# Kernel optimization log

Measured on AMD Instinct MI355X. Metric: run time of the kernel, lower is better.

The kernel has to match this reference:

```python
import jax, jax.numpy as jnp
import numpy as np

N = 8192       # tokens (batch*seq)
D = 4096       # input_size / d_model
H = 256        # gate hidden_size
E = 64         # num_experts
K = 2          # top_k


def setup_inputs() -> dict:
    key = jax.random.key(0)
    k0, k1, k2, k3 = jax.random.split(key, 4)
    x = jax.random.normal(k0, (N, D), dtype=jnp.float32)
    # nn.Linear default init: U(-1/sqrt(fan_in), 1/sqrt(fan_in))
    w1 = jax.random.uniform(k1, (H, D), jnp.float32, -1.0, 1.0) / np.sqrt(D)
    b1 = jax.random.uniform(k2, (H,), jnp.float32, -1.0, 1.0) / np.sqrt(D)
    w2 = jax.random.uniform(k3, (E, H), jnp.float32, -1.0, 1.0) / np.sqrt(H)
    return {"x": x, "w1": w1, "b1": b1, "w2": w2}


def reference(x, w1, b1, w2):
    # MLP gate: Linear -> GELU (exact erf, torch default) -> Dropout(eval: identity) -> Linear(no bias)
    h = jax.nn.gelu(jnp.einsum('nd,hd->nh', x, w1) + b1, approximate=False)  # [N, H]
    logits = jnp.einsum('nh,eh->ne', h, w2)                                  # [N, E]
    probs = jax.nn.softmax(logits, axis=-1)                                  # [N, E]
    # deterministic top-k path (sample_topk=0 / eval mode)
    top_k_gates, top_k_indices = jax.lax.top_k(probs, K)                     # [N, K] each
    return top_k_indices, top_k_gates, probs
```

## Files before the change

### kernel.cpp

```cpp
#include <hip/hip_runtime.h>
#include <hip/hip_bf16.h>
#include <math.h>

#define NTOK 8192
#define DIN  4096
#define HG   256
#define NE   64
#define SPLITK 4
#define KSTEPS 32
#define TR   16

typedef __attribute__((ext_vector_type(8))) short short8;
typedef __attribute__((ext_vector_type(4))) short short4v;
typedef __attribute__((ext_vector_type(4))) float f32x4;

__device__ __forceinline__ unsigned short f2bf_rne(float f) {
    union { float f; unsigned int u; } v; v.f = f;
    unsigned int r = v.u + 0x7fffu + ((v.u >> 16) & 1u);
    return (unsigned short)(r >> 16);
}
__device__ __forceinline__ float bf2f(unsigned short b) {
    union { unsigned int u; float f; } v; v.u = ((unsigned int)b) << 16;
    return v.f;
}

typedef const __attribute__((address_space(1))) unsigned int* gptr_t;
typedef __attribute__((address_space(3))) unsigned int* lptr_t;
__device__ __forceinline__ void gload_lds16(const void* g, void* l) {
    __builtin_amdgcn_global_load_lds((gptr_t)g, (lptr_t)l, 16, 0, 0);
}

__global__ __launch_bounds__(512) void convert_w1_kernel(
    const float* __restrict__ w1, unsigned short* __restrict__ w1t)
{
    const int id    = blockIdx.x * 512 + threadIdx.x;
    const int lane  = id & 63;
    const int cg    = id >> 6;
    const int kstep = cg >> 5;
    const int c     = cg & 31;
    const int hl    = c >> 4;
    const int unit  = c & 15;
    const int n     = unit * 16 + (lane & 15);
    const int k     = kstep * 32 + ((lane >> 4) & 3) * 8;

    const float* src = w1 + (size_t)n * DIN + k;
    short8 v;
#pragma unroll
    for (int j = 0; j < 8; ++j) {
        float f = src[j];
        unsigned short hi = f2bf_rne(f);
        v[j] = (hl == 0) ? (short)hi : (short)f2bf_rne(f - bf2f(hi));
    }
    *(short8*)(w1t + (size_t)cg * 512 + lane * 8) = v;
}

__global__ __launch_bounds__(256, 2) void gemm1_mfma_kernel(
    const float* __restrict__ x, const unsigned short* __restrict__ w1t,
    float* __restrict__ P)
{
    __shared__ unsigned short As[2][2][4][512];
    __shared__ unsigned short Bs[2][2][16][512];

    const int bid  = blockIdx.x;
    const int mblk = bid & 127;
    const int s    = bid >> 7;
    const int t    = threadIdx.x;
    const int lane = t & 63;
    const int w    = t >> 6;

    const int m_base = mblk * 64;
    const int kstep0 = s * KSTEPS;

    const int a_unit = t >> 6;
    const int a_q    = t & 63;
    const int a_row  = a_unit * 16 + (a_q & 15);
    const int a_koff = (a_q >> 4) * 8;
    const float* asrc = x + (size_t)(m_base + a_row) * DIN
                          + (size_t)kstep0 * 32 + a_koff;
    const int a_ldso = a_q * 8;

    f32x4 acc[4][4];
#pragma unroll
    for (int i = 0; i < 4; ++i)
#pragma unroll
        for (int j = 0; j < 4; ++j) acc[i][j] = (f32x4)0.f;

#define CVT8_STORE(BUF, F0, F1)                                               \
    {   short8 vh_, vl_;                                                      \
        float ff_[8] = { (F0).x, (F0).y, (F0).z, (F0).w,                      \
                         (F1).x, (F1).y, (F1).z, (F1).w };                    \
        _Pragma("unroll")                                                     \
        for (int j_ = 0; j_ < 8; ++j_) {                                      \
            unsigned short h_ = f2bf_rne(ff_[j_]);                            \
            vh_[j_] = (short)h_;                                              \
            vl_[j_] = (short)f2bf_rne(ff_[j_] - bf2f(h_));                    \
        }                                                                     \
        *(short8*)&As[BUF][0][a_unit][a_ldso] = vh_;                          \
        *(short8*)&As[BUF][1][a_unit][a_ldso] = vl_;                          \
    }

#pragma unroll
    for (int i = 0; i < 8; ++i) {
        const int c = w * 8 + i;
        gload_lds16(w1t + ((size_t)kstep0 * 32 + c) * 512 + lane * 8,
                    &Bs[0][c >> 4][c & 15][0]);
    }
    {
        float4 a0 = *(const float4*)(asrc);
        float4 a1 = *(const float4*)(asrc + 4);
        CVT8_STORE(0, a0, a1)
    }
    __syncthreads();

#pragma unroll 1
    for (int tt = 0; tt < KSTEPS; ++tt) {
        const int bcur = tt & 1, bnxt = bcur ^ 1;
        const bool last = (tt == KSTEPS - 1);

        float4 nx0, nx1;
        if (!last) {
            const float* ap = asrc + (size_t)(tt + 1) * 32;
            nx0 = *(const float4*)(ap);
            nx1 = *(const float4*)(ap + 4);
#pragma unroll
            for (int i = 0; i < 8; ++i) {
                const int c = w * 8 + i;
                gload_lds16(w1t + ((size_t)(kstep0 + tt + 1) * 32 + c) * 512 + lane * 8,
                            &Bs[bnxt][c >> 4][c & 15][0]);
            }
        }

        short8 ahf[4], alf[4], bhf[4], blf[4];
#pragma unroll
        for (int mr = 0; mr < 4; ++mr) {
            ahf[mr] = *(const short8*)&As[bcur][0][mr][lane * 8];
            alf[mr] = *(const short8*)&As[bcur][1][mr][lane * 8];
        }
#pragma unroll
        for (int nr = 0; nr < 4; ++nr) {
            bhf[nr] = *(const short8*)&Bs[bcur][0][w * 4 + nr][lane * 8];
            blf[nr] = *(const short8*)&Bs[bcur][1][w * 4 + nr][lane * 8];
        }

#pragma unroll
        for (int mr = 0; mr < 4; ++mr)
#pragma unroll
            for (int nr = 0; nr < 4; ++nr)
                acc[mr][nr] = __builtin_amdgcn_mfma_f32_16x16x32_bf16(
                    ahf[mr], bhf[nr], acc[mr][nr], 0, 0, 0);
#pragma unroll
        for (int mr = 0; mr < 4; ++mr)
#pragma unroll
            for (int nr = 0; nr < 4; ++nr)
                acc[mr][nr] = __builtin_amdgcn_mfma_f32_16x16x32_bf16(
                    ahf[mr], blf[nr], acc[mr][nr], 0, 0, 0);
#pragma unroll
        for (int mr = 0; mr < 4; ++mr)
#pragma unroll
            for (int nr = 0; nr < 4; ++nr)
                acc[mr][nr] = __builtin_amdgcn_mfma_f32_16x16x32_bf16(
                    alf[mr], bhf[nr], acc[mr][nr], 0, 0, 0);

        if (!last) {
            CVT8_STORE(bnxt, nx0, nx1)
            __syncthreads();
        }
    }
#undef CVT8_STORE

    float* pb = P + (size_t)s * ((size_t)NTOK * HG);
#pragma unroll
    for (int mr = 0; mr < 4; ++mr)
#pragma unroll
        for (int nr = 0; nr < 4; ++nr) {
            const int n = w * 64 + nr * 16 + (lane & 15);
#pragma unroll
            for (int r = 0; r < 4; ++r) {
                const int m = m_base + mr * 16 + ((lane >> 4) & 3) * 4 + r;
                pb[(size_t)m * HG + n] = acc[mr][nr][r];
            }
        }
}

__global__ __launch_bounds__(512, 4) void reduce_gate_kernel(
    const float* __restrict__ P, const float* __restrict__ b1,
    const float* __restrict__ w2, float* __restrict__ out)
{
    __shared__ float h_lds[TR][260];
    __shared__ float lg[NE][33];

    const int t    = threadIdx.x;
    const int lane = t & 63;
    const int w    = t >> 6;
    const int r0   = blockIdx.x * TR;
    const size_t SS = (size_t)NTOK * HG;

    {
        const int row = t >> 5;
        const int sg  = t & 31;
        const size_t base = (size_t)(r0 + row) * HG + sg * 8;

        float q[8];
#pragma unroll
        for (int half = 0; half < 2; ++half) {
            float4 v0 = *(const float4*)(P + base + half * 4);
            float4 v1 = *(const float4*)(P + base + SS + half * 4);
            float4 v2 = *(const float4*)(P + base + 2 * SS + half * 4);
            float4 v3 = *(const float4*)(P + base + 3 * SS + half * 4);
            float4 bb = *(const float4*)(b1 + sg * 8 + half * 4);
            q[half * 4 + 0] = v0.x + v1.x + v2.x + v3.x + bb.x;
            q[half * 4 + 1] = v0.y + v1.y + v2.y + v3.y + bb.y;
            q[half * 4 + 2] = v0.z + v1.z + v2.z + v3.z + bb.z;
            q[half * 4 + 3] = v0.w + v1.w + v2.w + v3.w + bb.w;
        }
#pragma unroll
        for (int c = 0; c < 8; ++c)
            q[c] = 0.5f * q[c] * (1.0f + erff(q[c] * 0.70710678118654752440f));

        *(float4*)&h_lds[row][sg * 8]     = make_float4(q[0], q[1], q[2], q[3]);
        *(float4*)&h_lds[row][sg * 8 + 4] = make_float4(q[4], q[5], q[6], q[7]);
    }
    __syncthreads();

    const int e0   = w * 8;
    const int rowp = lane & 15;
    const int kq   = lane >> 4;

    float acc[8];
#pragma unroll
    for (int i = 0; i < 8; ++i) acc[i] = 0.f;

    const float* w2b = w2 + (size_t)e0 * HG + kq * 64;
#pragma unroll 1
    for (int kc = 0; kc < 64; kc += 8) {
        float a[8];
        *(float4*)&a[0] = *(const float4*)&h_lds[rowp][kq * 64 + kc];
        *(float4*)&a[4] = *(const float4*)&h_lds[rowp][kq * 64 + kc + 4];
#pragma unroll
        for (int n = 0; n < 8; ++n) {
            const float* wr = w2b + (size_t)n * HG + kc;
            float4 w0 = *(const float4*)(wr);
            float4 w1v = *(const float4*)(wr + 4);
            acc[n] = fmaf(w0.x, a[0], acc[n]);
            acc[n] = fmaf(w0.y, a[1], acc[n]);
            acc[n] = fmaf(w0.z, a[2], acc[n]);
            acc[n] = fmaf(w0.w, a[3], acc[n]);
            acc[n] = fmaf(w1v.x, a[4], acc[n]);
            acc[n] = fmaf(w1v.y, a[5], acc[n]);
            acc[n] = fmaf(w1v.z, a[6], acc[n]);
            acc[n] = fmaf(w1v.w, a[7], acc[n]);
        }
    }
#pragma unroll
    for (int n = 0; n < 8; ++n) {
        acc[n] += __shfl_xor(acc[n], 16);
        acc[n] += __shfl_xor(acc[n], 32);
    }
    if (lane < 16) {
#pragma unroll
        for (int n = 0; n < 8; ++n) lg[e0 + n][rowp] = acc[n];
    }
    __syncthreads();

    if (t < TR) {
        float l[NE];
#pragma unroll
        for (int e = 0; e < NE; ++e) l[e] = lg[e][t];

        float mx = l[0];
#pragma unroll
        for (int e = 1; e < NE; ++e) mx = fmaxf(mx, l[e]);

        float ssum = 0.f;
#pragma unroll
        for (int e = 0; e < NE; ++e) { float p = expf(l[e] - mx); l[e] = p; ssum += p; }
        const float inv = 1.0f / ssum;
#pragma unroll
        for (int e = 0; e < NE; ++e) l[e] *= inv;

        float v1 = -1.0f, v2 = -2.0f;
        int   i1 = 0,     i2 = 0;
#pragma unroll
        for (int e = 0; e < NE; ++e) {
            const float p  = l[e];
            const bool  g1 = p > v1;
            const bool  g2 = p > v2;
            const float nv2 = g1 ? v1 : (g2 ? p : v2);
            const int   ni2 = g1 ? i1 : (g2 ? e : i2);
            v1 = g1 ? p : v1;
            i1 = g1 ? e : i1;
            v2 = nv2;
            i2 = ni2;
        }

        const int row = r0 + t;
        float* out_idx  = out;
        float* out_gate = out + 2 * NTOK;
        float* out_prob = out + 4 * NTOK;
        out_idx[2 * row + 0]  = (float)i1;
        out_idx[2 * row + 1]  = (float)i2;
        out_gate[2 * row + 0] = v1;
        out_gate[2 * row + 1] = v2;

        float* pr = out_prob + (size_t)row * NE;
#pragma unroll
        for (int e = 0; e < NE; e += 4)
            *(float4*)(pr + e) = make_float4(l[e], l[e + 1], l[e + 2], l[e + 3]);
    }
}

extern "C" void kernel_launch(void* const* d_in, const int* in_sizes, int n_in,
                              void* d_out, int out_size, void* d_ws, size_t ws_size,
                              hipStream_t stream) {
    const float* x  = (const float*)d_in[0];
    const float* w1 = (const float*)d_in[1];
    const float* b1 = (const float*)d_in[2];
    const float* w2 = (const float*)d_in[3];
    float* out = (float*)d_out;

    unsigned short* w1t = (unsigned short*)d_ws;
    float* P = (float*)((char*)d_ws + (4u << 20));

    convert_w1_kernel<<<512, 512, 0, stream>>>(w1, w1t);
    gemm1_mfma_kernel<<<512, 256, 0, stream>>>(x, w1t, P);
    reduce_gate_kernel<<<512, 512, 0, stream>>>(P, b1, w2, out);
}
```

Before: 91.77 us.

## Enlarge GEMM1 tile to 128 rows with 8 waves and triple-buffered W1 prefetch

The first GEMM now uses 512-thread blocks covering 128 token rows, so each W1 tile loaded into LDS feeds twice as many rows and B traffic drops. W1 tiles are triple-buffered and prefetched two k-steps ahead, with explicit vmcnt waits and raw barriers in place of __syncthreads. Blocks are remapped so neighbouring blocks share a split-K slice, and MFMA sections run at raised wave priority. The cost is more LDS per block and half as many blocks (256), which may reduce occupancy and latency hiding on a device with many CUs.

```diff
diff --git a/kernel.cpp b/kernel.cpp
--- a/kernel.cpp
+++ b/kernel.cpp
@@ -11,7 +11,6 @@
 #define TR   16
 
 typedef __attribute__((ext_vector_type(8))) short short8;
-typedef __attribute__((ext_vector_type(4))) short short4v;
 typedef __attribute__((ext_vector_type(4))) float f32x4;
 
 __device__ __forceinline__ unsigned short f2bf_rne(float f) {
@@ -29,6 +28,13 @@
 __device__ __forceinline__ void gload_lds16(const void* g, void* l) {
     __builtin_amdgcn_global_load_lds((gptr_t)g, (lptr_t)l, 16, 0, 0);
 }
+
+#define WAIT_VMCNT4 { asm volatile("s_waitcnt vmcnt(4)" ::: "memory"); \
+                      __builtin_amdgcn_sched_barrier(0); }
+#define WAIT_VMCNT0 { asm volatile("s_waitcnt vmcnt(0)" ::: "memory"); \
+                      __builtin_amdgcn_sched_barrier(0); }
+#define WAIT_LGKM0  { asm volatile("s_waitcnt lgkmcnt(0)" ::: "memory"); \
+                      __builtin_amdgcn_sched_barrier(0); }
 
 __global__ __launch_bounds__(512) void convert_w1_kernel(
     const float* __restrict__ w1, unsigned short* __restrict__ w1t)
@@ -54,21 +60,23 @@
     *(short8*)(w1t + (size_t)cg * 512 + lane * 8) = v;
 }
 
-__global__ __launch_bounds__(256, 2) void gemm1_mfma_kernel(
+__global__ __launch_bounds__(512, 2) void gemm1_mfma_kernel(
     const float* __restrict__ x, const unsigned short* __restrict__ w1t,
     float* __restrict__ P)
 {
-    __shared__ unsigned short As[2][2][4][512];
-    __shared__ unsigned short Bs[2][2][16][512];
+    __shared__ unsigned short As[2][2][8][512];
+    __shared__ unsigned short Bs[3][2][16][512];
 
     const int bid  = blockIdx.x;
-    const int mblk = bid & 127;
-    const int s    = bid >> 7;
+    const int s    = (bid & 7) >> 1;
+    const int mblk = ((bid >> 3) << 1) | (bid & 1);
     const int t    = threadIdx.x;
     const int lane = t & 63;
     const int w    = t >> 6;
-
-    const int m_base = mblk * 64;
+    const int wm   = w >> 2;
+    const int wn   = w & 3;
+
+    const int m_base = mblk * 128;
     const int kstep0 = s * KSTEPS;
 
     const int a_unit = t >> 6;
@@ -99,49 +107,54 @@
         *(short8*)&As[BUF][1][a_unit][a_ldso] = vl_;                          \
     }
 
-#pragma unroll
-    for (int i = 0; i < 8; ++i) {
-        const int c = w * 8 + i;
-        gload_lds16(w1t + ((size_t)kstep0 * 32 + c) * 512 + lane * 8,
-                    &Bs[0][c >> 4][c & 15][0]);
-    }
+#define ISSUE_B(KS, BUF)                                                      \
+    _Pragma("unroll")                                                         \
+    for (int i_ = 0; i_ < 4; ++i_) {                                          \
+        const int c_ = w * 4 + i_;                                            \
+        gload_lds16(w1t + ((size_t)(KS) * 32 + c_) * 512 + lane * 8,          \
+                    &Bs[BUF][c_ >> 4][c_ & 15][0]);                           \
+    }
+
     {
         float4 a0 = *(const float4*)(asrc);
         float4 a1 = *(const float4*)(asrc + 4);
+        ISSUE_B(kstep0, 0)
         CVT8_STORE(0, a0, a1)
-    }
-    __syncthreads();
+        ISSUE_B(kstep0 + 1, 1)
+        WAIT_VMCNT4
+        WAIT_LGKM0
+        __builtin_amdgcn_s_barrier();
+    }
+
+    int bcur = 0, bnx1 = 1, bnx2 = 2;
+    int acur = 0;
 
 #pragma unroll 1
     for (int tt = 0; tt < KSTEPS; ++tt) {
-        const int bcur = tt & 1, bnxt = bcur ^ 1;
-        const bool last = (tt == KSTEPS - 1);
+        const bool has1 = (tt + 1 < KSTEPS);
+        const bool has2 = (tt + 2 < KSTEPS);
 
         float4 nx0, nx1;
-        if (!last) {
+        if (has1) {
             const float* ap = asrc + (size_t)(tt + 1) * 32;
             nx0 = *(const float4*)(ap);
             nx1 = *(const float4*)(ap + 4);
-#pragma unroll
-            for (int i = 0; i < 8; ++i) {
-                const int c = w * 8 + i;
-                gload_lds16(w1t + ((size_t)(kstep0 + tt + 1) * 32 + c) * 512 + lane * 8,
-                            &Bs[bnxt][c >> 4][c & 15][0]);
-            }
-        }
+        }
+        if (has2) { ISSUE_B(kstep0 + tt + 2, bnx2) }
 
         short8 ahf[4], alf[4], bhf[4], blf[4];
 #pragma unroll
         for (int mr = 0; mr < 4; ++mr) {
-            ahf[mr] = *(const short8*)&As[bcur][0][mr][lane * 8];
-            alf[mr] = *(const short8*)&As[bcur][1][mr][lane * 8];
+            ahf[mr] = *(const short8*)&As[acur][0][wm * 4 + mr][lane * 8];
+            alf[mr] = *(const short8*)&As[acur][1][wm * 4 + mr][lane * 8];
         }
 #pragma unroll
         for (int nr = 0; nr < 4; ++nr) {
-            bhf[nr] = *(const short8*)&Bs[bcur][0][w * 4 + nr][lane * 8];
-            blf[nr] = *(const short8*)&Bs[bcur][1][w * 4 + nr][lane * 8];
-        }
-
+            bhf[nr] = *(const short8*)&Bs[bcur][0][wn * 4 + nr][lane * 8];
+            blf[nr] = *(const short8*)&Bs[bcur][1][wn * 4 + nr][lane * 8];
+        }
+
+        __builtin_amdgcn_s_setprio(1);
 #pragma unroll
         for (int mr = 0; mr < 4; ++mr)
 #pragma unroll
@@ -160,12 +173,20 @@
             for (int nr = 0; nr < 4; ++nr)
                 acc[mr][nr] = __builtin_amdgcn_mfma_f32_16x16x32_bf16(
                     alf[mr], bhf[nr], acc[mr][nr], 0, 0, 0);
-
-        if (!last) {
-            CVT8_STORE(bnxt, nx0, nx1)
-            __syncthreads();
-        }
-    }
+        __builtin_amdgcn_s_setprio(0);
+
+        if (has1) {
+            CVT8_STORE(acur ^ 1, nx0, nx1)
+            if (has2) { WAIT_VMCNT4 }
+            else      { WAIT_VMCNT0 }
+            WAIT_LGKM0
+            __builtin_amdgcn_s_barrier();
+        }
+
+        const int z = bcur; bcur = bnx1; bnx1 = bnx2; bnx2 = z;
+        acur ^= 1;
+    }
+#undef ISSUE_B
 #undef CVT8_STORE
 
     float* pb = P + (size_t)s * ((size_t)NTOK * HG);
@@ -173,10 +194,10 @@
     for (int mr = 0; mr < 4; ++mr)
 #pragma unroll
         for (int nr = 0; nr < 4; ++nr) {
-            const int n = w * 64 + nr * 16 + (lane & 15);
+            const int n = wn * 64 + nr * 16 + (lane & 15);
 #pragma unroll
             for (int r = 0; r < 4; ++r) {
-                const int m = m_base + mr * 16 + ((lane >> 4) & 3) * 4 + r;
+                const int m = m_base + wm * 64 + mr * 16 + ((lane >> 4) & 3) * 4 + r;
                 pb[(size_t)m * HG + n] = acc[mr][nr][r];
             }
         }
@@ -322,6 +343,6 @@
     float* P = (float*)((char*)d_ws + (4u << 20));
 
     convert_w1_kernel<<<512, 512, 0, stream>>>(w1, w1t);
-    gemm1_mfma_kernel<<<512, 256, 0, stream>>>(x, w1t, P);
+    gemm1_mfma_kernel<<<256, 512, 0, stream>>>(x, w1t, P);
     reduce_gate_kernel<<<512, 512, 0, stream>>>(P, b1, w2, out);
 }
```

Measured after the change: 104.3 us. 13.6% more time.
